# Kernel tuning notes

Hardware: AMD Instinct MI355X
Metric: run time of the kernel (lower is better)

Reference implementation:

```python
import jax, jax.numpy as jnp
import numpy as np

N_NODES = 50000
N_HEDGES = 10000
NNZ_INC = 400000
NNZ_E = 80000
NNZ_V = 400000
VDIM = 128
EDIM = 128
OUT_VDIM = 128
OUT_EDIM = 128


def _spmm(rows, cols, vals, X, n_rows):
    # sparse COO [n_rows, n_cols] @ X  -> [n_rows, d]
    return jax.ops.segment_sum(vals[:, None] * X[cols], rows, num_segments=n_rows)


def setup_inputs() -> dict:
    key = jax.random.key(0)
    ks = jax.random.split(key, 20)
    inp = {
        "vfeat": jax.random.normal(ks[0], (N_NODES, VDIM), jnp.float32),
        "efeat": jax.random.normal(ks[1], (N_HEDGES, EDIM), jnp.float32),
        "invDV": jax.random.uniform(ks[2], (N_NODES,), jnp.float32),
        "invDE": jax.random.uniform(ks[3], (N_HEDGES,), jnp.float32),
        "inc_src": jax.random.randint(ks[4], (NNZ_INC,), 0, N_NODES, jnp.int32),
        "inc_dst": jax.random.randint(ks[5], (NNZ_INC,), 0, N_HEDGES, jnp.int32),
        "emat_rows": jax.random.randint(ks[6], (NNZ_E,), 0, N_HEDGES, jnp.int32),
        "emat_cols": jax.random.randint(ks[7], (NNZ_E,), 0, N_HEDGES, jnp.int32),
        "emat_vals": jax.random.normal(ks[8], (NNZ_E,), jnp.float32),
        "vmat_rows": jax.random.randint(ks[9], (NNZ_V,), 0, N_NODES, jnp.int32),
        "vmat_cols": jax.random.randint(ks[10], (NNZ_V,), 0, N_NODES, jnp.int32),
        "vmat_vals": jax.random.normal(ks[11], (NNZ_V,), jnp.float32),
        # parameters (torch Linear: y = x @ W.T + b)
        "Wv": jax.random.normal(ks[12], (OUT_VDIM, VDIM), jnp.float32) * 0.05,
        "We": jax.random.normal(ks[13], (OUT_EDIM, EDIM), jnp.float32) * 0.05,
        "psi1_W": jax.random.normal(ks[14], (VDIM, VDIM + EDIM), jnp.float32) * 0.05,
        "psi1_b": jnp.zeros((VDIM,), jnp.float32),
        "psi2_W": jax.random.normal(ks[15], (EDIM, OUT_VDIM + EDIM), jnp.float32) * 0.05,
        "psi2_b": jnp.zeros((EDIM,), jnp.float32),
    }
    return inp


def reference(vfeat, efeat, invDV, invDE, inc_src, inc_dst,
              emat_rows, emat_cols, emat_vals,
              vmat_rows, vmat_cols, vmat_vals,
              Wv, We, psi1_W, psi1_b, psi2_W, psi2_b):
    N = vfeat.shape[0]
    E = efeat.shape[0]
    # --- 'in' update_all with psi1: per-incidence concat -> linear -> *invDV[src] -> sum into hyperedge
    x = jnp.concatenate([vfeat[inc_src], efeat[inc_dst]], axis=1)  # [nnz, VDIM+EDIM]
    x = x @ psi1_W.T + psi1_b                                       # [nnz, VDIM]
    x = x * invDV[inc_src][:, None]
    A = jax.ops.segment_sum(x, inc_dst, num_segments=E)             # [E, VDIM]
    A = _spmm(emat_rows, emat_cols, emat_vals, A, E)
    _efeat = A + efeat
    # --- 'con' update_all: node gathers sum of incident hyperedge feats
    _vfeat = jax.ops.segment_sum(_efeat[inc_dst], inc_src, num_segments=N)
    vfeat_out = jax.nn.relu(_vfeat @ Wv.T)                           # [N, OUT_VDIM]
    # --- 'in' update_all with psi2 (dv = ones)
    x2 = jnp.concatenate([vfeat_out[inc_src], efeat[inc_dst]], axis=1)
    x2 = x2 @ psi2_W.T + psi2_b                                      # [nnz, EDIM]
    B = jax.ops.segment_sum(x2, inc_dst, num_segments=E) * invDE[:, None]
    # --- 'con' pass with efeat, then vMat spmm, then 'in' sum back to hyperedges
    _vfeat2 = jax.ops.segment_sum(efeat[inc_dst], inc_src, num_segments=N)
    _vfeat2 = _spmm(vmat_rows, vmat_cols, vmat_vals, _vfeat2, N)
    _efeat2 = jax.ops.segment_sum(_vfeat2[inc_src], inc_dst, num_segments=E)
    _efeat2 = _efeat2 + B
    efeat_out = jax.nn.relu(_efeat2 @ We.T)                          # [E, OUT_EDIM]
    return vfeat_out, efeat_out
```

## Files before the change

kernel.cpp:

```cpp
#include <hip/hip_runtime.h>

#define NN 50000
#define NE 10000
#define NNZ_INC 400000
#define NNZ_E 80000
#define NNZ_V 400000
#define D 128
#define KC 32

#define CAP_D 112
#define CAP_S 40
#define CAP_E 40
#define CAP_V 40

#define GN_ 782
#define GE_ 157
#define G_HINC ((NNZ_INC + 255) / 256)
#define G_EV ((NNZ_E + NNZ_V + 255) / 256)
#define G_CVTN 6250
#define G_CVTE 1250
#define G_NR16 (NN / 16)
#define G_ER16 (NE / 16)

typedef unsigned short u16;
typedef unsigned int u32;

__device__ __forceinline__ u16 f2bf(float x) {
    unsigned u = __float_as_uint(x);
    unsigned r = u + 0x7fffu + ((u >> 16) & 1u);
    return (u16)(r >> 16);
}
__device__ __forceinline__ float bf2f(u16 h) {
    return __uint_as_float(((unsigned)h) << 16);
}

__device__ __forceinline__ void acc8(uint4 u, float acc[8]) {
    acc[0] += __uint_as_float(u.x << 16);
    acc[1] += __uint_as_float(u.x & 0xffff0000u);
    acc[2] += __uint_as_float(u.y << 16);
    acc[3] += __uint_as_float(u.y & 0xffff0000u);
    acc[4] += __uint_as_float(u.z << 16);
    acc[5] += __uint_as_float(u.z & 0xffff0000u);
    acc[6] += __uint_as_float(u.w << 16);
    acc[7] += __uint_as_float(u.w & 0xffff0000u);
}
__device__ __forceinline__ void fma8(uint4 u, float v, float acc[8]) {
    acc[0] = fmaf(v, __uint_as_float(u.x << 16), acc[0]);
    acc[1] = fmaf(v, __uint_as_float(u.x & 0xffff0000u), acc[1]);
    acc[2] = fmaf(v, __uint_as_float(u.y << 16), acc[2]);
    acc[3] = fmaf(v, __uint_as_float(u.y & 0xffff0000u), acc[3]);
    acc[4] = fmaf(v, __uint_as_float(u.z << 16), acc[4]);
    acc[5] = fmaf(v, __uint_as_float(u.z & 0xffff0000u), acc[5]);
    acc[6] = fmaf(v, __uint_as_float(u.w << 16), acc[6]);
    acc[7] = fmaf(v, __uint_as_float(u.w & 0xffff0000u), acc[7]);
}
__device__ __forceinline__ uint4 pack_bf8(const float acc[8]) {
    uint4 o;
    o.x = (u32)f2bf(acc[0]) | ((u32)f2bf(acc[1]) << 16);
    o.y = (u32)f2bf(acc[2]) | ((u32)f2bf(acc[3]) << 16);
    o.z = (u32)f2bf(acc[4]) | ((u32)f2bf(acc[5]) << 16);
    o.w = (u32)f2bf(acc[6]) | ((u32)f2bf(acc[7]) << 16);
    return o;
}

__device__ __forceinline__ void gemm_acc(
    int bx, const float* __restrict__ X, const float* __restrict__ W, int ldw,
    int M, float acc[8][4])
{
    __shared__ float XsT[KC][68];
    __shared__ float Ws[KC][132];
    const int tid = threadIdx.x;
    const int tx = tid & 31, ty = tid >> 5;
    const int row0 = bx * 64;
    const int c0 = tx * 4;
    const int r0 = ty * 8;

#pragma unroll
    for (int r = 0; r < 8; ++r)
#pragma unroll
        for (int c = 0; c < 4; ++c) acc[r][c] = 0.f;

    for (int kc = 0; kc < D; kc += KC) {
        __syncthreads();
#pragma unroll
        for (int it = 0; it < 2; ++it) {
            int l = tid + it * 256;
            int r = l >> 3, k4 = l & 7;
            float4 v = make_float4(0.f, 0.f, 0.f, 0.f);
            int row = row0 + r;
            if (row < M) v = ((const float4*)(X + (size_t)row * D + kc))[k4];
            int k = k4 * 4;
            XsT[k + 0][r] = v.x; XsT[k + 1][r] = v.y;
            XsT[k + 2][r] = v.z; XsT[k + 3][r] = v.w;
        }
#pragma unroll
        for (int it = 0; it < 4; ++it) {
            int l = tid + it * 256;
            int o = l >> 3, k4 = l & 7;
            float4 w = ((const float4*)(W + (size_t)o * ldw + kc))[k4];
            int k = k4 * 4;
            Ws[k + 0][o] = w.x; Ws[k + 1][o] = w.y;
            Ws[k + 2][o] = w.z; Ws[k + 3][o] = w.w;
        }
        __syncthreads();
#pragma unroll
        for (int k = 0; k < KC; ++k) {
            const float4 a0 = *(const float4*)&XsT[k][r0];
            const float4 a1 = *(const float4*)&XsT[k][r0 + 4];
            const float4 b  = *(const float4*)&Ws[k][c0];
            float av[8] = {a0.x, a0.y, a0.z, a0.w, a1.x, a1.y, a1.z, a1.w};
            float bv[4] = {b.x, b.y, b.z, b.w};
#pragma unroll
            for (int r = 0; r < 8; ++r)
#pragma unroll
                for (int c = 0; c < 4; ++c)
                    acc[r][c] = fmaf(av[r], bv[c], acc[r][c]);
        }
    }
}

__device__ __forceinline__ void gemm_acc2(
    int bx, const float* __restrict__ X1, const float* __restrict__ X2,
    const float* __restrict__ rsf, const int* __restrict__ rsi,
    const float* __restrict__ W, int M, float acc[8][4])
{
    __shared__ float XsT[KC][68];
    __shared__ float Ws[KC][132];
    const int tid = threadIdx.x;
    const int tx = tid & 31, ty = tid >> 5;
    const int row0 = bx * 64;
    const int c0 = tx * 4;
    const int r0 = ty * 8;

#pragma unroll
    for (int r = 0; r < 8; ++r)
#pragma unroll
        for (int c = 0; c < 4; ++c) acc[r][c] = 0.f;

    for (int kc = 0; kc < 2 * D; kc += KC) {
        __syncthreads();
        const bool second = (kc >= D);
        const float* Xp = second ? X2 : X1;
        const int kk = second ? kc - D : kc;
#pragma unroll
        for (int it = 0; it < 2; ++it) {
            int l = tid + it * 256;
            int r = l >> 3, k4 = l & 7;
            float4 v = make_float4(0.f, 0.f, 0.f, 0.f);
            int row = row0 + r;
            if (row < M) {
                v = ((const float4*)(Xp + (size_t)row * D + kk))[k4];
                if (second) {
                    float sc = rsf ? rsf[row] : (float)rsi[row];
                    v.x *= sc; v.y *= sc; v.z *= sc; v.w *= sc;
                }
            }
            int k = k4 * 4;
            XsT[k + 0][r] = v.x; XsT[k + 1][r] = v.y;
            XsT[k + 2][r] = v.z; XsT[k + 3][r] = v.w;
        }
#pragma unroll
        for (int it = 0; it < 4; ++it) {
            int l = tid + it * 256;
            int o = l >> 3, k4 = l & 7;
            float4 w = ((const float4*)(W + (size_t)o * (2 * D) + kc))[k4];
            int k = k4 * 4;
            Ws[k + 0][o] = w.x; Ws[k + 1][o] = w.y;
            Ws[k + 2][o] = w.z; Ws[k + 3][o] = w.w;
        }
        __syncthreads();
#pragma unroll
        for (int k = 0; k < KC; ++k) {
            const float4 a0 = *(const float4*)&XsT[k][r0];
            const float4 a1 = *(const float4*)&XsT[k][r0 + 4];
            const float4 b  = *(const float4*)&Ws[k][c0];
            float av[8] = {a0.x, a0.y, a0.z, a0.w, a1.x, a1.y, a1.z, a1.w};
            float bv[4] = {b.x, b.y, b.z, b.w};
#pragma unroll
            for (int r = 0; r < 8; ++r)
#pragma unroll
                for (int c = 0; c < 4; ++c)
                    acc[r][c] = fmaf(av[r], bv[c], acc[r][c]);
        }
    }
}

__global__ __launch_bounds__(256) void mega0(
    const int* __restrict__ inc_src, const int* __restrict__ inc_dst,
    int* __restrict__ cnt_dst, int* __restrict__ cnt_src,
    u16* __restrict__ ell_d, u16* __restrict__ ell_s,
    const float* __restrict__ efeat, const float* __restrict__ vfeat,
    const float* __restrict__ invDV,
    u16* __restrict__ vfi_b, u16* __restrict__ efeat_b)
{
    int b = blockIdx.x;
    if (b < G_HINC) {
        int i = b * 256 + threadIdx.x;
        if (i < NNZ_INC) {
            int s = inc_src[i], d = inc_dst[i];
            int rd = atomicAdd(cnt_dst + d, 1);
            if (rd < CAP_D) ell_d[d * CAP_D + rd] = (u16)s;
            int rs = atomicAdd(cnt_src + s, 1);
            if (rs < CAP_S) ell_s[s * CAP_S + rs] = (u16)d;
        }
    } else if (b < G_HINC + G_CVTN) {
        int i = ((b - G_HINC) * 256 + threadIdx.x) * 4;
        int row = i >> 7;
        float s = invDV[row];
        float4 v = *(const float4*)(vfeat + i);
        ushort4 u;
        u.x = f2bf(v.x * s); u.y = f2bf(v.y * s);
        u.z = f2bf(v.z * s); u.w = f2bf(v.w * s);
        *(ushort4*)(vfi_b + i) = u;
    } else {
        int i = ((b - G_HINC - G_CVTN) * 256 + threadIdx.x) * 4;
        float4 v = *(const float4*)(efeat + i);
        ushort4 u;
        u.x = f2bf(v.x); u.y = f2bf(v.y); u.z = f2bf(v.z); u.w = f2bf(v.w);
        *(ushort4*)(efeat_b + i) = u;
    }
}

__device__ __forceinline__ void segsum_bf_ell16(int rb,
    const int* __restrict__ cnt, int cap, const u16* __restrict__ ell,
    const u16* __restrict__ Tb, u16* __restrict__ Yb, int R)
{
    int r = rb * 16 + (threadIdx.x >> 4);
    int q = threadIdx.x & 15;
    if (r >= R) return;
    int m = min(cnt[r], cap);
    const u16* lst = ell + (size_t)r * cap;
    float acc[8] = {0.f, 0.f, 0.f, 0.f, 0.f, 0.f, 0.f, 0.f};
    int j = 0;
    for (; j + 3 < m; j += 4) {
        ushort4 ix = *(const ushort4*)(lst + j);
        uint4 u0 = *(const uint4*)(Tb + (size_t)ix.x * D + q * 8);
        uint4 u1 = *(const uint4*)(Tb + (size_t)ix.y * D + q * 8);
        uint4 u2 = *(const uint4*)(Tb + (size_t)ix.z * D + q * 8);
        uint4 u3 = *(const uint4*)(Tb + (size_t)ix.w * D + q * 8);
        acc8(u0, acc); acc8(u1, acc); acc8(u2, acc); acc8(u3, acc);
    }
    for (; j < m; ++j) {
        uint4 u0 = *(const uint4*)(Tb + (size_t)lst[j] * D + q * 8);
        acc8(u0, acc);
    }
    ((uint4*)(Yb + (size_t)r * D))[q] = pack_bf8(acc);
}

__device__ __forceinline__ void segsum_f_ell16(int rb,
    const int* __restrict__ cnt, int cap, const u16* __restrict__ ell,
    const u16* __restrict__ Tb, float* __restrict__ Y, int R)
{
    int r = rb * 16 + (threadIdx.x >> 4);
    int q = threadIdx.x & 15;
    if (r >= R) return;
    int m = min(cnt[r], cap);
    const u16* lst = ell + (size_t)r * cap;
    float acc[8] = {0.f, 0.f, 0.f, 0.f, 0.f, 0.f, 0.f, 0.f};
    int j = 0;
    for (; j + 3 < m; j += 4) {
        ushort4 ix = *(const ushort4*)(lst + j);
        uint4 u0 = *(const uint4*)(Tb + (size_t)ix.x * D + q * 8);
        uint4 u1 = *(const uint4*)(Tb + (size_t)ix.y * D + q * 8);
        uint4 u2 = *(const uint4*)(Tb + (size_t)ix.z * D + q * 8);
        uint4 u3 = *(const uint4*)(Tb + (size_t)ix.w * D + q * 8);
        acc8(u0, acc); acc8(u1, acc); acc8(u2, acc); acc8(u3, acc);
    }
    for (; j < m; ++j) {
        uint4 u0 = *(const uint4*)(Tb + (size_t)lst[j] * D + q * 8);
        acc8(u0, acc);
    }
    float* yr = Y + (size_t)r * D;
    ((float4*)yr)[2 * q + 0] = make_float4(acc[0], acc[1], acc[2], acc[3]);
    ((float4*)yr)[2 * q + 1] = make_float4(acc[4], acc[5], acc[6], acc[7]);
}

__device__ __forceinline__ void spmm_bf_ell16(int rb,
    const int* __restrict__ cnt, int cap, const u32* __restrict__ ell,
    const u16* __restrict__ Xb, const float* __restrict__ addend,
    u16* __restrict__ Yb, int R)
{
    int r = rb * 16 + (threadIdx.x >> 4);
    int q = threadIdx.x & 15;
    if (r >= R) return;
    int m = min(cnt[r], cap);
    const u32* lst = ell + (size_t)r * cap;
    float acc[8];
    if (addend) {
        const float* ar = addend + (size_t)r * D;
        float4 lo = ((const float4*)ar)[2 * q + 0];
        float4 hi = ((const float4*)ar)[2 * q + 1];
        acc[0] = lo.x; acc[1] = lo.y; acc[2] = lo.z; acc[3] = lo.w;
        acc[4] = hi.x; acc[5] = hi.y; acc[6] = hi.z; acc[7] = hi.w;
    } else {
#pragma unroll
        for (int i = 0; i < 8; ++i) acc[i] = 0.f;
    }
    int j = 0;
    for (; j + 3 < m; j += 4) {
        uint4 e = *(const uint4*)(lst + j);
        uint4 x0 = *(const uint4*)(Xb + (size_t)(e.x >> 16) * D + q * 8);
        uint4 x1 = *(const uint4*)(Xb + (size_t)(e.y >> 16) * D + q * 8);
        uint4 x2 = *(const uint4*)(Xb + (size_t)(e.z >> 16) * D + q * 8);
        uint4 x3 = *(const uint4*)(Xb + (size_t)(e.w >> 16) * D + q * 8);
        fma8(x0, __uint_as_float(e.x << 16), acc);
        fma8(x1, __uint_as_float(e.y << 16), acc);
        fma8(x2, __uint_as_float(e.z << 16), acc);
        fma8(x3, __uint_as_float(e.w << 16), acc);
    }
    for (; j < m; ++j) {
        u32 e = lst[j];
        uint4 x = *(const uint4*)(Xb + (size_t)(e >> 16) * D + q * 8);
        fma8(x, __uint_as_float(e << 16), acc);
    }
    ((uint4*)(Yb + (size_t)r * D))[q] = pack_bf8(acc);
}

__global__ __launch_bounds__(256) void fusedA(
    const int* __restrict__ erows, const int* __restrict__ ecols,
    const float* __restrict__ evals, int* __restrict__ cnt_e, u32* __restrict__ ev_e,
    const int* __restrict__ vrows, const int* __restrict__ vcols,
    const float* __restrict__ vvals, int* __restrict__ cnt_v, u32* __restrict__ ev_v,
    const int* __restrict__ cnt_dst, const u16* __restrict__ ell_d,
    const float* __restrict__ invDV, const u16* __restrict__ vfi_b,
    float* __restrict__ sva, float* __restrict__ wsum,
    const int* __restrict__ cnt_src, const u16* __restrict__ ell_s,
    const u16* __restrict__ efeat_b, u16* __restrict__ vf2_b)
{
    int b = blockIdx.x;
    if (b < G_EV) {
        int i = b * 256 + threadIdx.x;
        if (i < NNZ_E) {
            int r = erows[i];
            int re = atomicAdd(cnt_e + r, 1);
            if (re < CAP_E)
                ev_e[r * CAP_E + re] = ((u32)ecols[i] << 16) | (u32)f2bf(evals[i]);
        } else if (i < NNZ_E + NNZ_V) {
            int j = i - NNZ_E;
            int r = vrows[j];
            int rv = atomicAdd(cnt_v + r, 1);
            if (rv < CAP_V)
                ev_v[r * CAP_V + rv] = ((u32)vcols[j] << 16) | (u32)f2bf(vvals[j]);
        }
    } else if (b < G_EV + G_ER16) {
        int e = (b - G_EV) * 16 + (threadIdx.x >> 4);
        int q = threadIdx.x & 15;
        if (e >= NE) return;
        int m = min(cnt_dst[e], CAP_D);
        const u16* lst = ell_d + (size_t)e * CAP_D;
        float acc[8] = {0.f, 0.f, 0.f, 0.f, 0.f, 0.f, 0.f, 0.f};
        float ws = 0.f;
        int j = 0;
        for (; j + 3 < m; j += 4) {
            ushort4 ix = *(const ushort4*)(lst + j);
            uint4 u0 = *(const uint4*)(vfi_b + (size_t)ix.x * D + q * 8);
            uint4 u1 = *(const uint4*)(vfi_b + (size_t)ix.y * D + q * 8);
            uint4 u2 = *(const uint4*)(vfi_b + (size_t)ix.z * D + q * 8);
            uint4 u3 = *(const uint4*)(vfi_b + (size_t)ix.w * D + q * 8);
            ws += (invDV[ix.x] + invDV[ix.y]) + (invDV[ix.z] + invDV[ix.w]);
            acc8(u0, acc); acc8(u1, acc); acc8(u2, acc); acc8(u3, acc);
        }
        for (; j < m; ++j) {
            int s = lst[j];
            uint4 u0 = *(const uint4*)(vfi_b + (size_t)s * D + q * 8);
            ws += invDV[s];
            acc8(u0, acc);
        }
        float* yr = sva + (size_t)e * D;
        ((float4*)yr)[2 * q + 0] = make_float4(acc[0], acc[1], acc[2], acc[3]);
        ((float4*)yr)[2 * q + 1] = make_float4(acc[4], acc[5], acc[6], acc[7]);
        if (q == 0) wsum[e] = ws;
    } else {
        segsum_bf_ell16(b - G_EV - G_ER16, cnt_src, CAP_S, ell_s, efeat_b, vf2_b, NN);
    }
}

__global__ __launch_bounds__(256) void gemmA_k(
    const float* __restrict__ sva, const float* __restrict__ efeat,
    const float* __restrict__ wsum,
    const float* __restrict__ psi1_W, const float* __restrict__ psi1_b,
    u16* __restrict__ A_b)
{
    float acc[8][4];
    gemm_acc2(blockIdx.x, sva, efeat, wsum, nullptr, psi1_W, NE, acc);
    int tx = threadIdx.x & 31, ty = threadIdx.x >> 5;
    float4 b4 = ((const float4*)psi1_b)[tx];
#pragma unroll
    for (int r = 0; r < 8; ++r) {
        int row = blockIdx.x * 64 + ty * 8 + r;
        if (row < NE) {
            float ws = wsum[row];
            ushort4 u;
            u.x = f2bf(fmaf(ws, b4.x, acc[r][0]));
            u.y = f2bf(fmaf(ws, b4.y, acc[r][1]));
            u.z = f2bf(fmaf(ws, b4.z, acc[r][2]));
            u.w = f2bf(fmaf(ws, b4.w, acc[r][3]));
            ((ushort4*)(A_b + (size_t)row * D))[tx] = u;
        }
    }
}

__global__ __launch_bounds__(256) void fusedB(
    const int* __restrict__ cnt_e, const u32* __restrict__ ev_e,
    const u16* __restrict__ A_b, const float* __restrict__ efeat, u16* __restrict__ A2_b,
    const int* __restrict__ cnt_v, const u32* __restrict__ ev_v,
    const u16* __restrict__ vf2_b, u16* __restrict__ vf2b_b)
{
    int b = blockIdx.x;
    if (b < G_ER16) spmm_bf_ell16(b, cnt_e, CAP_E, ev_e, A_b, efeat, A2_b, NE);
    else spmm_bf_ell16(b - G_ER16, cnt_v, CAP_V, ev_v, vf2_b, nullptr, vf2b_b, NN);
}

__global__ __launch_bounds__(256) void fusedD(
    const int* __restrict__ cnt_src, const u16* __restrict__ ell_s,
    const u16* __restrict__ A2_b, float* __restrict__ vf1)
{
    segsum_f_ell16(blockIdx.x, cnt_src, CAP_S, ell_s, A2_b, vf1, NN);
}

__global__ __launch_bounds__(256) void gemmC_k(
    const float* __restrict__ vf1, const float* __restrict__ Wv,
    float* __restrict__ out_v, u16* __restrict__ outv_b)
{
    float acc[8][4];
    gemm_acc(blockIdx.x, vf1, Wv, D, NN, acc);
    int tx = threadIdx.x & 31, ty = threadIdx.x >> 5;
#pragma unroll
    for (int r = 0; r < 8; ++r) {
        int row = blockIdx.x * 64 + ty * 8 + r;
        if (row < NN) {
            float4 v = make_float4(fmaxf(acc[r][0], 0.f), fmaxf(acc[r][1], 0.f),
                                   fmaxf(acc[r][2], 0.f), fmaxf(acc[r][3], 0.f));
            ((float4*)(out_v + (size_t)row * D))[tx] = v;
            ushort4 u;
            u.x = f2bf(v.x); u.y = f2bf(v.y); u.z = f2bf(v.z); u.w = f2bf(v.w);
            ((ushort4*)(outv_b + (size_t)row * D))[tx] = u;
        }
    }
}

__global__ __launch_bounds__(256) void gather_avsv(
    const int* __restrict__ cnt_dst, const u16* __restrict__ ell_d,
    const u16* __restrict__ vf2b_b, const u16* __restrict__ outv_b,
    float* __restrict__ av, float* __restrict__ sv)
{
    int r = blockIdx.x * 16 + (threadIdx.x >> 4);
    int q = threadIdx.x & 15;
    if (r >= NE) return;
    int m = min(cnt_dst[r], CAP_D);
    const u16* lst = ell_d + (size_t)r * CAP_D;
    float a[8] = {0.f, 0.f, 0.f, 0.f, 0.f, 0.f, 0.f, 0.f};
    float s[8] = {0.f, 0.f, 0.f, 0.f, 0.f, 0.f, 0.f, 0.f};
    int j = 0;
    for (; j + 1 < m; j += 2) {
        ushort2 ix = *(const ushort2*)(lst + j);
        uint4 a0 = *(const uint4*)(vf2b_b + (size_t)ix.x * D + q * 8);
        uint4 a1 = *(const uint4*)(vf2b_b + (size_t)ix.y * D + q * 8);
        uint4 s0 = *(const uint4*)(outv_b + (size_t)ix.x * D + q * 8);
        uint4 s1 = *(const uint4*)(outv_b + (size_t)ix.y * D + q * 8);
        acc8(a0, a); acc8(a1, a);
        acc8(s0, s); acc8(s1, s);
    }
    for (; j < m; ++j) {
        int ix = lst[j];
        uint4 a0 = *(const uint4*)(vf2b_b + (size_t)ix * D + q * 8);
        uint4 s0 = *(const uint4*)(outv_b + (size_t)ix * D + q * 8);
        acc8(a0, a); acc8(s0, s);
    }
    float* ar = av + (size_t)r * D;
    ((float4*)ar)[2 * q + 0] = make_float4(a[0], a[1], a[2], a[3]);
    ((float4*)ar)[2 * q + 1] = make_float4(a[4], a[5], a[6], a[7]);
    float* sr = sv + (size_t)r * D;
    ((float4*)sr)[2 * q + 0] = make_float4(s[0], s[1], s[2], s[3]);
    ((float4*)sr)[2 * q + 1] = make_float4(s[4], s[5], s[6], s[7]);
}

__global__ __launch_bounds__(256) void gemmBE_k(
    const float* __restrict__ sv, const float* __restrict__ efeat,
    const int* __restrict__ cnt_dst,
    const float* __restrict__ psi2_W, const float* __restrict__ psi2_b,
    const float* __restrict__ invDE, const float* __restrict__ av,
    const float* __restrict__ We, float* __restrict__ out_e)
{
    __shared__ float T[D][68];
    float acc[8][4];
    gemm_acc2(blockIdx.x, sv, efeat, nullptr, cnt_dst, psi2_W, NE, acc);
    const int tx = threadIdx.x & 31, ty = threadIdx.x >> 5;
    const int bx = blockIdx.x;
    float4 b2 = ((const float4*)psi2_b)[tx];
#pragma unroll
    for (int r = 0; r < 8; ++r) {
        int row = bx * 64 + ty * 8 + r;
        float deg = 0.f, ide = 0.f;
        float4 a = make_float4(0.f, 0.f, 0.f, 0.f);
        if (row < NE) {
            deg = (float)cnt_dst[row];
            ide = invDE[row];
            a = ((const float4*)(av + (size_t)row * D))[tx];
        }
        int lr = ty * 8 + r;
        T[tx * 4 + 0][lr] = fmaf(deg, b2.x, acc[r][0]) * ide + a.x;
        T[tx * 4 + 1][lr] = fmaf(deg, b2.y, acc[r][1]) * ide + a.y;
        T[tx * 4 + 2][lr] = fmaf(deg, b2.z, acc[r][2]) * ide + a.z;
        T[tx * 4 + 3][lr] = fmaf(deg, b2.w, acc[r][3]) * ide + a.w;
    }
    __shared__ float Ws2[KC][132];
    float acc2[8][4];
#pragma unroll
    for (int r = 0; r < 8; ++r)
#pragma unroll
        for (int c = 0; c < 4; ++c) acc2[r][c] = 0.f;
    const int c0 = tx * 4, r0 = ty * 8;
    for (int kc = 0; kc < D; kc += KC) {
        __syncthreads();
#pragma unroll
        for (int it = 0; it < 4; ++it) {
            int l = threadIdx.x + it * 256;
            int o = l >> 3, k4 = l & 7;
            float4 w = ((const float4*)(We + (size_t)o * D + kc))[k4];
            int k = k4 * 4;
            Ws2[k + 0][o] = w.x; Ws2[k + 1][o] = w.y;
            Ws2[k + 2][o] = w.z; Ws2[k + 3][o] = w.w;
        }
        __syncthreads();
#pragma unroll
        for (int k = 0; k < KC; ++k) {
            const float4 a0 = *(const float4*)&T[kc + k][r0];
            const float4 a1 = *(const float4*)&T[kc + k][r0 + 4];
            const float4 bb = *(const float4*)&Ws2[k][c0];
            float avv[8] = {a0.x, a0.y, a0.z, a0.w, a1.x, a1.y, a1.z, a1.w};
            float bv[4] = {bb.x, bb.y, bb.z, bb.w};
#pragma unroll
            for (int r = 0; r < 8; ++r)
#pragma unroll
                for (int c = 0; c < 4; ++c)
                    acc2[r][c] = fmaf(avv[r], bv[c], acc2[r][c]);
        }
    }
#pragma unroll
    for (int r = 0; r < 8; ++r) {
        int row = bx * 64 + ty * 8 + r;
        if (row < NE) {
            float4 v = make_float4(fmaxf(acc2[r][0], 0.f), fmaxf(acc2[r][1], 0.f),
                                   fmaxf(acc2[r][2], 0.f), fmaxf(acc2[r][3], 0.f));
            ((float4*)(out_e + (size_t)row * D))[tx] = v;
        }
    }
}

extern "C" void kernel_launch(void* const* d_in, const int* in_sizes, int n_in,
                              void* d_out, int out_size, void* d_ws, size_t ws_size,
                              hipStream_t stream)
{
    (void)in_sizes; (void)n_in; (void)out_size; (void)ws_size;
    const float* vfeat     = (const float*)d_in[0];
    const float* efeat     = (const float*)d_in[1];
    const float* invDV     = (const float*)d_in[2];
    const float* invDE     = (const float*)d_in[3];
    const int*   inc_src   = (const int*)d_in[4];
    const int*   inc_dst   = (const int*)d_in[5];
    const int*   emat_rows = (const int*)d_in[6];
    const int*   emat_cols = (const int*)d_in[7];
    const float* emat_vals = (const float*)d_in[8];
    const int*   vmat_rows = (const int*)d_in[9];
    const int*   vmat_cols = (const int*)d_in[10];
    const float* vmat_vals = (const float*)d_in[11];
    const float* Wv        = (const float*)d_in[12];
    const float* We        = (const float*)d_in[13];
    const float* psi1_W    = (const float*)d_in[14];
    const float* psi1_b    = (const float*)d_in[15];
    const float* psi2_W    = (const float*)d_in[16];
    const float* psi2_b    = (const float*)d_in[17];

    const size_t ND = (size_t)NN * D;
    const size_t ED = (size_t)NE * D;

    char* p = (char*)d_ws;
    auto alloc = [&](size_t bytes) {
        size_t a = (size_t)p; a = (a + 255) & ~(size_t)255;
        p = (char*)a; void* r = (void*)p; p += bytes; return r;
    };
    float* vf1   = (float*)alloc(ND * 4);
    float* av    = (float*)alloc(ED * 4);
    float* svbuf = (float*)alloc(ED * 4);
    float* wsum  = (float*)alloc((size_t)NE * 4);
    u16* vfi_b   = (u16*)alloc(ND * 2);
    u16* outv_b  = (u16*)alloc(ND * 2);
    u16* vf2_b   = (u16*)alloc(ND * 2);
    u16* vf2b_b  = (u16*)alloc(ND * 2);
    u16* efeat_b = (u16*)alloc(ED * 2);
    u16* A_b     = (u16*)alloc(ED * 2);
    u16* A2_b    = (u16*)alloc(ED * 2);
    int* cnt_dst = (int*)alloc((size_t)(2 * NE + 2 * NN) * 4);
    int* cnt_src = cnt_dst + NE;
    int* cnt_e   = cnt_src + NN;
    int* cnt_v   = cnt_e + NE;
    u16* ell_d   = (u16*)alloc((size_t)NE * CAP_D * 2);
    u16* ell_s   = (u16*)alloc((size_t)NN * CAP_S * 2);
    u32* ev_e    = (u32*)alloc((size_t)NE * CAP_E * 4);
    u32* ev_v    = (u32*)alloc((size_t)NN * CAP_V * 4);

    float* out_v = (float*)d_out;
    float* out_e = out_v + ND;

    dim3 b256(256);

    hipMemsetAsync(cnt_dst, 0, (size_t)(2 * NE + 2 * NN) * sizeof(int), stream);
    mega0<<<G_HINC + G_CVTN + G_CVTE, b256, 0, stream>>>(
        inc_src, inc_dst, cnt_dst, cnt_src, ell_d, ell_s,
        efeat, vfeat, invDV, vfi_b, efeat_b);
    fusedA<<<G_EV + G_ER16 + G_NR16, b256, 0, stream>>>(
        emat_rows, emat_cols, emat_vals, cnt_e, ev_e,
        vmat_rows, vmat_cols, vmat_vals, cnt_v, ev_v,
        cnt_dst, ell_d, invDV, vfi_b, svbuf, wsum,
        cnt_src, ell_s, efeat_b, vf2_b);
    gemmA_k<<<GE_, b256, 0, stream>>>(svbuf, efeat, wsum, psi1_W, psi1_b, A_b);
    fusedB<<<G_ER16 + G_NR16, b256, 0, stream>>>(
        cnt_e, ev_e, A_b, efeat, A2_b,
        cnt_v, ev_v, vf2_b, vf2b_b);
    fusedD<<<G_NR16, b256, 0, stream>>>(cnt_src, ell_s, A2_b, vf1);
    gemmC_k<<<GN_, b256, 0, stream>>>(vf1, Wv, out_v, outv_b);
    gather_avsv<<<G_ER16, b256, 0, stream>>>(
        cnt_dst, ell_d, vf2b_b, outv_b, av, svbuf);
    gemmBE_k<<<GE_, b256, 0, stream>>>(
        svbuf, efeat, cnt_dst, psi2_W, psi2_b, invDE, av, We, out_e);
}
```

Measured before the change: 387.1 us.

## Reassociate psi2 linear before gather, shard incidence histogram, regroup kernels

Result: slower. 408.2 us (+5.5%).

```diff
diff --git a/kernel.cpp b/kernel.cpp
--- a/kernel.cpp
+++ b/kernel.cpp
@@ -13,9 +13,13 @@
 #define CAP_E 40
 #define CAP_V 40
 
+#define NE_SH (NE / 8)
+#define NN_SH (NN / 8)
+
 #define GN_ 782
 #define GE_ 157
 #define G_HINC ((NNZ_INC + 255) / 256)
+#define G_HIST8 (8 * G_HINC)
 #define G_EV ((NNZ_E + NNZ_V + 255) / 256)
 #define G_CVTN 6250
 #define G_CVTE 1250
@@ -121,7 +125,7 @@
 
 __device__ __forceinline__ void gemm_acc2(
     int bx, const float* __restrict__ X1, const float* __restrict__ X2,
-    const float* __restrict__ rsf, const int* __restrict__ rsi,
+    const float* __restrict__ rsf,
     const float* __restrict__ W, int M, float acc[8][4])
 {
     __shared__ float XsT[KC][68];
@@ -151,7 +155,7 @@
             if (row < M) {
                 v = ((const float4*)(Xp + (size_t)row * D + kk))[k4];
                 if (second) {
-                    float sc = rsf ? rsf[row] : (float)rsi[row];
+                    float sc = rsf[row];
                     v.x *= sc; v.y *= sc; v.z *= sc; v.w *= sc;
                 }
             }
@@ -194,17 +198,22 @@
     u16* __restrict__ vfi_b, u16* __restrict__ efeat_b)
 {
     int b = blockIdx.x;
-    if (b < G_HINC) {
-        int i = b * 256 + threadIdx.x;
+    if (b < G_HIST8) {
+        int shard = b & 7;
+        int i = (b >> 3) * 256 + threadIdx.x;
         if (i < NNZ_INC) {
             int s = inc_src[i], d = inc_dst[i];
-            int rd = atomicAdd(cnt_dst + d, 1);
-            if (rd < CAP_D) ell_d[d * CAP_D + rd] = (u16)s;
-            int rs = atomicAdd(cnt_src + s, 1);
-            if (rs < CAP_S) ell_s[s * CAP_S + rs] = (u16)d;
-        }
-    } else if (b < G_HINC + G_CVTN) {
-        int i = ((b - G_HINC) * 256 + threadIdx.x) * 4;
+            if ((u32)(d - shard * NE_SH) < (u32)NE_SH) {
+                int rd = atomicAdd(cnt_dst + d, 1);
+                if (rd < CAP_D) ell_d[d * CAP_D + rd] = (u16)s;
+            }
+            if ((u32)(s - shard * NN_SH) < (u32)NN_SH) {
+                int rs = atomicAdd(cnt_src + s, 1);
+                if (rs < CAP_S) ell_s[s * CAP_S + rs] = (u16)d;
+            }
+        }
+    } else if (b < G_HIST8 + G_CVTN) {
+        int i = ((b - G_HIST8) * 256 + threadIdx.x) * 4;
         int row = i >> 7;
         float s = invDV[row];
         float4 v = *(const float4*)(vfeat + i);
@@ -213,7 +222,7 @@
         u.z = f2bf(v.z * s); u.w = f2bf(v.w * s);
         *(ushort4*)(vfi_b + i) = u;
     } else {
-        int i = ((b - G_HINC - G_CVTN) * 256 + threadIdx.x) * 4;
+        int i = ((b - G_HIST8 - G_CVTN) * 256 + threadIdx.x) * 4;
         float4 v = *(const float4*)(efeat + i);
         ushort4 u;
         u.x = f2bf(v.x); u.y = f2bf(v.y); u.z = f2bf(v.z); u.w = f2bf(v.w);
@@ -321,6 +330,8 @@
     const float* __restrict__ evals, int* __restrict__ cnt_e, u32* __restrict__ ev_e,
     const int* __restrict__ vrows, const int* __restrict__ vcols,
     const float* __restrict__ vvals, int* __restrict__ cnt_v, u32* __restrict__ ev_v,
+    const float* __restrict__ efeat,
+    const float* __restrict__ psi2_W, const float* __restrict__ psi2_b, float* __restrict__ QeP,
     const int* __restrict__ cnt_dst, const u16* __restrict__ ell_d,
     const float* __restrict__ invDV, const u16* __restrict__ vfi_b,
     float* __restrict__ sva, float* __restrict__ wsum,
@@ -342,8 +353,23 @@
             if (rv < CAP_V)
                 ev_v[r * CAP_V + rv] = ((u32)vcols[j] << 16) | (u32)f2bf(vvals[j]);
         }
-    } else if (b < G_EV + G_ER16) {
-        int e = (b - G_EV) * 16 + (threadIdx.x >> 4);
+    } else if (b < G_EV + GE_) {
+        int bx = b - G_EV;
+        float acc[8][4];
+        gemm_acc(bx, efeat, psi2_W + D, 2 * D, NE, acc);
+        int tx = threadIdx.x & 31, ty = threadIdx.x >> 5;
+        float4 b4 = ((const float4*)psi2_b)[tx];
+#pragma unroll
+        for (int r = 0; r < 8; ++r) {
+            int row = bx * 64 + ty * 8 + r;
+            if (row < NE) {
+                float4 v = make_float4(acc[r][0] + b4.x, acc[r][1] + b4.y,
+                                       acc[r][2] + b4.z, acc[r][3] + b4.w);
+                ((float4*)(QeP + (size_t)row * D))[tx] = v;
+            }
+        }
+    } else if (b < G_EV + GE_ + G_ER16) {
+        int e = (b - G_EV - GE_) * 16 + (threadIdx.x >> 4);
         int q = threadIdx.x & 15;
         if (e >= NE) return;
         int m = min(cnt_dst[e], CAP_D);
@@ -371,138 +397,81 @@
         ((float4*)yr)[2 * q + 1] = make_float4(acc[4], acc[5], acc[6], acc[7]);
         if (q == 0) wsum[e] = ws;
     } else {
-        segsum_bf_ell16(b - G_EV - G_ER16, cnt_src, CAP_S, ell_s, efeat_b, vf2_b, NN);
-    }
-}
-
-__global__ __launch_bounds__(256) void gemmA_k(
+        segsum_bf_ell16(b - G_EV - GE_ - G_ER16, cnt_src, CAP_S, ell_s, efeat_b, vf2_b, NN);
+    }
+}
+
+__global__ __launch_bounds__(256) void fusedB2(
     const float* __restrict__ sva, const float* __restrict__ efeat,
     const float* __restrict__ wsum,
     const float* __restrict__ psi1_W, const float* __restrict__ psi1_b,
-    u16* __restrict__ A_b)
-{
-    float acc[8][4];
-    gemm_acc2(blockIdx.x, sva, efeat, wsum, nullptr, psi1_W, NE, acc);
-    int tx = threadIdx.x & 31, ty = threadIdx.x >> 5;
-    float4 b4 = ((const float4*)psi1_b)[tx];
-#pragma unroll
-    for (int r = 0; r < 8; ++r) {
-        int row = blockIdx.x * 64 + ty * 8 + r;
-        if (row < NE) {
-            float ws = wsum[row];
-            ushort4 u;
-            u.x = f2bf(fmaf(ws, b4.x, acc[r][0]));
-            u.y = f2bf(fmaf(ws, b4.y, acc[r][1]));
-            u.z = f2bf(fmaf(ws, b4.z, acc[r][2]));
-            u.w = f2bf(fmaf(ws, b4.w, acc[r][3]));
-            ((ushort4*)(A_b + (size_t)row * D))[tx] = u;
-        }
-    }
-}
-
-__global__ __launch_bounds__(256) void fusedB(
+    u16* __restrict__ A_b,
+    const int* __restrict__ cnt_v, const u32* __restrict__ ev_v,
+    const u16* __restrict__ vf2_b, u16* __restrict__ vf2b_b)
+{
+    int b = blockIdx.x;
+    if (b < GE_) {
+        float acc[8][4];
+        gemm_acc2(b, sva, efeat, wsum, psi1_W, NE, acc);
+        int tx = threadIdx.x & 31, ty = threadIdx.x >> 5;
+        float4 b4 = ((const float4*)psi1_b)[tx];
+#pragma unroll
+        for (int r = 0; r < 8; ++r) {
+            int row = b * 64 + ty * 8 + r;
+            if (row < NE) {
+                float ws = wsum[row];
+                ushort4 u;
+                u.x = f2bf(fmaf(ws, b4.x, acc[r][0]));
+                u.y = f2bf(fmaf(ws, b4.y, acc[r][1]));
+                u.z = f2bf(fmaf(ws, b4.z, acc[r][2]));
+                u.w = f2bf(fmaf(ws, b4.w, acc[r][3]));
+                ((ushort4*)(A_b + (size_t)row * D))[tx] = u;
+            }
+        }
+    } else {
+        spmm_bf_ell16(b - GE_, cnt_v, CAP_V, ev_v, vf2_b, nullptr, vf2b_b, NN);
+    }
+}
+
+__global__ __launch_bounds__(256) void fusedC2(
     const int* __restrict__ cnt_e, const u32* __restrict__ ev_e,
     const u16* __restrict__ A_b, const float* __restrict__ efeat, u16* __restrict__ A2_b,
-    const int* __restrict__ cnt_v, const u32* __restrict__ ev_v,
-    const u16* __restrict__ vf2_b, u16* __restrict__ vf2b_b)
+    const int* __restrict__ cnt_dst, const u16* __restrict__ ell_d,
+    const u16* __restrict__ vf2b_b, float* __restrict__ av)
 {
     int b = blockIdx.x;
     if (b < G_ER16) spmm_bf_ell16(b, cnt_e, CAP_E, ev_e, A_b, efeat, A2_b, NE);
-    else spmm_bf_ell16(b - G_ER16, cnt_v, CAP_V, ev_v, vf2_b, nullptr, vf2b_b, NN);
-}
-
-__global__ __launch_bounds__(256) void fusedD(
+    else segsum_f_ell16(b - G_ER16, cnt_dst, CAP_D, ell_d, vf2b_b, av, NE);
+}
+
+__global__ __launch_bounds__(256) void fusedD2(
     const int* __restrict__ cnt_src, const u16* __restrict__ ell_s,
     const u16* __restrict__ A2_b, float* __restrict__ vf1)
 {
     segsum_f_ell16(blockIdx.x, cnt_src, CAP_S, ell_s, A2_b, vf1, NN);
 }
 
-__global__ __launch_bounds__(256) void gemmC_k(
+__global__ __launch_bounds__(256) void gemmC2_k(
     const float* __restrict__ vf1, const float* __restrict__ Wv,
-    float* __restrict__ out_v, u16* __restrict__ outv_b)
-{
+    const float* __restrict__ psi2_W,
+    float* __restrict__ out_v, u16* __restrict__ Z_b)
+{
+    __shared__ float T[D][68];
     float acc[8][4];
     gemm_acc(blockIdx.x, vf1, Wv, D, NN, acc);
-    int tx = threadIdx.x & 31, ty = threadIdx.x >> 5;
-#pragma unroll
-    for (int r = 0; r < 8; ++r) {
-        int row = blockIdx.x * 64 + ty * 8 + r;
-        if (row < NN) {
-            float4 v = make_float4(fmaxf(acc[r][0], 0.f), fmaxf(acc[r][1], 0.f),
-                                   fmaxf(acc[r][2], 0.f), fmaxf(acc[r][3], 0.f));
-            ((float4*)(out_v + (size_t)row * D))[tx] = v;
-            ushort4 u;
-            u.x = f2bf(v.x); u.y = f2bf(v.y); u.z = f2bf(v.z); u.w = f2bf(v.w);
-            ((ushort4*)(outv_b + (size_t)row * D))[tx] = u;
-        }
-    }
-}
-
-__global__ __launch_bounds__(256) void gather_avsv(
-    const int* __restrict__ cnt_dst, const u16* __restrict__ ell_d,
-    const u16* __restrict__ vf2b_b, const u16* __restrict__ outv_b,
-    float* __restrict__ av, float* __restrict__ sv)
-{
-    int r = blockIdx.x * 16 + (threadIdx.x >> 4);
-    int q = threadIdx.x & 15;
-    if (r >= NE) return;
-    int m = min(cnt_dst[r], CAP_D);
-    const u16* lst = ell_d + (size_t)r * CAP_D;
-    float a[8] = {0.f, 0.f, 0.f, 0.f, 0.f, 0.f, 0.f, 0.f};
-    float s[8] = {0.f, 0.f, 0.f, 0.f, 0.f, 0.f, 0.f, 0.f};
-    int j = 0;
-    for (; j + 1 < m; j += 2) {
-        ushort2 ix = *(const ushort2*)(lst + j);
-        uint4 a0 = *(const uint4*)(vf2b_b + (size_t)ix.x * D + q * 8);
-        uint4 a1 = *(const uint4*)(vf2b_b + (size_t)ix.y * D + q * 8);
-        uint4 s0 = *(const uint4*)(outv_b + (size_t)ix.x * D + q * 8);
-        uint4 s1 = *(const uint4*)(outv_b + (size_t)ix.y * D + q * 8);
-        acc8(a0, a); acc8(a1, a);
-        acc8(s0, s); acc8(s1, s);
-    }
-    for (; j < m; ++j) {
-        int ix = lst[j];
-        uint4 a0 = *(const uint4*)(vf2b_b + (size_t)ix * D + q * 8);
-        uint4 s0 = *(const uint4*)(outv_b + (size_t)ix * D + q * 8);
-        acc8(a0, a); acc8(s0, s);
-    }
-    float* ar = av + (size_t)r * D;
-    ((float4*)ar)[2 * q + 0] = make_float4(a[0], a[1], a[2], a[3]);
-    ((float4*)ar)[2 * q + 1] = make_float4(a[4], a[5], a[6], a[7]);
-    float* sr = sv + (size_t)r * D;
-    ((float4*)sr)[2 * q + 0] = make_float4(s[0], s[1], s[2], s[3]);
-    ((float4*)sr)[2 * q + 1] = make_float4(s[4], s[5], s[6], s[7]);
-}
-
-__global__ __launch_bounds__(256) void gemmBE_k(
-    const float* __restrict__ sv, const float* __restrict__ efeat,
-    const int* __restrict__ cnt_dst,
-    const float* __restrict__ psi2_W, const float* __restrict__ psi2_b,
-    const float* __restrict__ invDE, const float* __restrict__ av,
-    const float* __restrict__ We, float* __restrict__ out_e)
-{
-    __shared__ float T[D][68];
-    float acc[8][4];
-    gemm_acc2(blockIdx.x, sv, efeat, nullptr, cnt_dst, psi2_W, NE, acc);
     const int tx = threadIdx.x & 31, ty = threadIdx.x >> 5;
     const int bx = blockIdx.x;
-    float4 b2 = ((const float4*)psi2_b)[tx];
 #pragma unroll
     for (int r = 0; r < 8; ++r) {
         int row = bx * 64 + ty * 8 + r;
-        float deg = 0.f, ide = 0.f;
-        float4 a = make_float4(0.f, 0.f, 0.f, 0.f);
-        if (row < NE) {
-            deg = (float)cnt_dst[row];
-            ide = invDE[row];
-            a = ((const float4*)(av + (size_t)row * D))[tx];
-        }
+        float4 v = make_float4(fmaxf(acc[r][0], 0.f), fmaxf(acc[r][1], 0.f),
+                               fmaxf(acc[r][2], 0.f), fmaxf(acc[r][3], 0.f));
+        if (row < NN) ((float4*)(out_v + (size_t)row * D))[tx] = v;
         int lr = ty * 8 + r;
-        T[tx * 4 + 0][lr] = fmaf(deg, b2.x, acc[r][0]) * ide + a.x;
-        T[tx * 4 + 1][lr] = fmaf(deg, b2.y, acc[r][1]) * ide + a.y;
-        T[tx * 4 + 2][lr] = fmaf(deg, b2.z, acc[r][2]) * ide + a.z;
-        T[tx * 4 + 3][lr] = fmaf(deg, b2.w, acc[r][3]) * ide + a.w;
+        T[tx * 4 + 0][lr] = v.x;
+        T[tx * 4 + 1][lr] = v.y;
+        T[tx * 4 + 2][lr] = v.z;
+        T[tx * 4 + 3][lr] = v.w;
     }
     __shared__ float Ws2[KC][132];
     float acc2[8][4];
@@ -517,7 +486,7 @@
         for (int it = 0; it < 4; ++it) {
             int l = threadIdx.x + it * 256;
             int o = l >> 3, k4 = l & 7;
-            float4 w = ((const float4*)(We + (size_t)o * D + kc))[k4];
+            float4 w = ((const float4*)(psi2_W + (size_t)o * (2 * D) + kc))[k4];
             int k = k4 * 4;
             Ws2[k + 0][o] = w.x; Ws2[k + 1][o] = w.y;
             Ws2[k + 2][o] = w.z; Ws2[k + 3][o] = w.w;
@@ -540,9 +509,76 @@
 #pragma unroll
     for (int r = 0; r < 8; ++r) {
         int row = bx * 64 + ty * 8 + r;
+        if (row < NN) {
+            ushort4 u;
+            u.x = f2bf(acc2[r][0]); u.y = f2bf(acc2[r][1]);
+            u.z = f2bf(acc2[r][2]); u.w = f2bf(acc2[r][3]);
+            ((ushort4*)(Z_b + (size_t)row * D))[tx] = u;
+        }
+    }
+}
+
+__global__ __launch_bounds__(256) void gatherZ_k(
+    const int* __restrict__ cnt_dst, const u16* __restrict__ ell_d,
+    const u16* __restrict__ Z_b,
+    const float* __restrict__ QeP, const float* __restrict__ invDE,
+    const float* __restrict__ av, float* __restrict__ ef2)
+{
+    int r = blockIdx.x * 16 + (threadIdx.x >> 4);
+    int q = threadIdx.x & 15;
+    if (r >= NE) return;
+    int cd = cnt_dst[r];
+    int m = min(cd, CAP_D);
+    const u16* lst = ell_d + (size_t)r * CAP_D;
+    float acc[8] = {0.f, 0.f, 0.f, 0.f, 0.f, 0.f, 0.f, 0.f};
+    int j = 0;
+    for (; j + 3 < m; j += 4) {
+        ushort4 ix = *(const ushort4*)(lst + j);
+        uint4 u0 = *(const uint4*)(Z_b + (size_t)ix.x * D + q * 8);
+        uint4 u1 = *(const uint4*)(Z_b + (size_t)ix.y * D + q * 8);
+        uint4 u2 = *(const uint4*)(Z_b + (size_t)ix.z * D + q * 8);
+        uint4 u3 = *(const uint4*)(Z_b + (size_t)ix.w * D + q * 8);
+        acc8(u0, acc); acc8(u1, acc); acc8(u2, acc); acc8(u3, acc);
+    }
+    for (; j < m; ++j) {
+        uint4 u0 = *(const uint4*)(Z_b + (size_t)lst[j] * D + q * 8);
+        acc8(u0, acc);
+    }
+    float deg = (float)cd;
+    float ide = invDE[r];
+    const float* qp = QeP + (size_t)r * D;
+    const float* ap = av + (size_t)r * D;
+    float4 q0 = ((const float4*)qp)[2 * q + 0];
+    float4 q1 = ((const float4*)qp)[2 * q + 1];
+    float4 a0 = ((const float4*)ap)[2 * q + 0];
+    float4 a1 = ((const float4*)ap)[2 * q + 1];
+    float4 o0, o1;
+    o0.x = fmaf(deg, q0.x, acc[0]) * ide + a0.x;
+    o0.y = fmaf(deg, q0.y, acc[1]) * ide + a0.y;
+    o0.z = fmaf(deg, q0.z, acc[2]) * ide + a0.z;
+    o0.w = fmaf(deg, q0.w, acc[3]) * ide + a0.w;
+    o1.x = fmaf(deg, q1.x, acc[4]) * ide + a1.x;
+    o1.y = fmaf(deg, q1.y, acc[5]) * ide + a1.y;
+    o1.z = fmaf(deg, q1.z, acc[6]) * ide + a1.z;
+    o1.w = fmaf(deg, q1.w, acc[7]) * ide + a1.w;
+    float* yr = ef2 + (size_t)r * D;
+    ((float4*)yr)[2 * q + 0] = o0;
+    ((float4*)yr)[2 * q + 1] = o1;
+}
+
+__global__ __launch_bounds__(256) void gemmE_k(
+    const float* __restrict__ ef2, const float* __restrict__ We,
+    float* __restrict__ out_e)
+{
+    float acc[8][4];
+    gemm_acc(blockIdx.x, ef2, We, D, NE, acc);
+    int tx = threadIdx.x & 31, ty = threadIdx.x >> 5;
+#pragma unroll
+    for (int r = 0; r < 8; ++r) {
+        int row = blockIdx.x * 64 + ty * 8 + r;
         if (row < NE) {
-            float4 v = make_float4(fmaxf(acc2[r][0], 0.f), fmaxf(acc2[r][1], 0.f),
-                                   fmaxf(acc2[r][2], 0.f), fmaxf(acc2[r][3], 0.f));
+            float4 v = make_float4(fmaxf(acc[r][0], 0.f), fmaxf(acc[r][1], 0.f),
+                                   fmaxf(acc[r][2], 0.f), fmaxf(acc[r][3], 0.f));
             ((float4*)(out_e + (size_t)row * D))[tx] = v;
         }
     }
@@ -580,12 +616,13 @@
         size_t a = (size_t)p; a = (a + 255) & ~(size_t)255;
         p = (char*)a; void* r = (void*)p; p += bytes; return r;
     };
+    float* QeP   = (float*)alloc(ED * 4);
     float* vf1   = (float*)alloc(ND * 4);
     float* av    = (float*)alloc(ED * 4);
     float* svbuf = (float*)alloc(ED * 4);
     float* wsum  = (float*)alloc((size_t)NE * 4);
     u16* vfi_b   = (u16*)alloc(ND * 2);
-    u16* outv_b  = (u16*)alloc(ND * 2);
+    u16* Z_b     = (u16*)alloc(ND * 2);
     u16* vf2_b   = (u16*)alloc(ND * 2);
     u16* vf2b_b  = (u16*)alloc(ND * 2);
     u16* efeat_b = (u16*)alloc(ED * 2);
@@ -606,22 +643,24 @@
     dim3 b256(256);
 
     hipMemsetAsync(cnt_dst, 0, (size_t)(2 * NE + 2 * NN) * sizeof(int), stream);
-    mega0<<<G_HINC + G_CVTN + G_CVTE, b256, 0, stream>>>(
+    mega0<<<G_HIST8 + G_CVTN + G_CVTE, b256, 0, stream>>>(
         inc_src, inc_dst, cnt_dst, cnt_src, ell_d, ell_s,
         efeat, vfeat, invDV, vfi_b, efeat_b);
-    fusedA<<<G_EV + G_ER16 + G_NR16, b256, 0, stream>>>(
+    fusedA<<<G_EV + GE_ + G_ER16 + G_NR16, b256, 0, stream>>>(
         emat_rows, emat_cols, emat_vals, cnt_e, ev_e,
         vmat_rows, vmat_cols, vmat_vals, cnt_v, ev_v,
+        efeat, psi2_W, psi2_b, QeP,
         cnt_dst, ell_d, invDV, vfi_b, svbuf, wsum,
         cnt_src, ell_s, efeat_b, vf2_b);
-    gemmA_k<<<GE_, b256, 0, stream>>>(svbuf, efeat, wsum, psi1_W, psi1_b, A_b);
-    fusedB<<<G_ER16 + G_NR16, b256, 0, stream>>>(
+    fusedB2<<<GE_ + G_NR16, b256, 0, stream>>>(
+        svbuf, efeat, wsum, psi1_W, psi1_b, A_b,
+        cnt_v, ev_v, vf2_b, vf2b_b);
+    fusedC2<<<G_ER16 + G_ER16, b256, 0, stream>>>(
         cnt_e, ev_e, A_b, efeat, A2_b,
-        cnt_v, ev_v, vf2_b, vf2b_b);
-    fusedD<<<G_NR16, b256, 0, stream>>>(cnt_src, ell_s, A2_b, vf1);
-    gemmC_k<<<GN_, b256, 0, stream>>>(vf1, Wv, out_v, outv_b);
-    gather_avsv<<<G_ER16, b256, 0, stream>>>(
-        cnt_dst, ell_d, vf2b_b, outv_b, av, svbuf);
-    gemmBE_k<<<GE_, b256, 0, stream>>>(
-        svbuf, efeat, cnt_dst, psi2_W, psi2_b, invDE, av, We, out_e);
-}
+        cnt_dst, ell_d, vf2b_b, av);
+    fusedD2<<<G_NR16, b256, 0, stream>>>(cnt_src, ell_s, A2_b, vf1);
+    gemmC2_k<<<GN_, b256, 0, stream>>>(vf1, Wv, psi2_W, out_v, Z_b);
+    gatherZ_k<<<G_ER16, b256, 0, stream>>>(
+        cnt_dst, ell_d, Z_b, QeP, invDE, av, svbuf);
+    gemmE_k<<<GE_, b256, 0, stream>>>(svbuf, We, out_e);
+}
```
